# Kernel tuning notes

Hardware: AMD Instinct MI355X
Metric: run time of the kernel (lower is better)

Reference implementation:

```python
import jax, jax.numpy as jnp
import numpy as np
from math import gcd


def _get_start_index(length):
    if length <= 2:
        return 0
    return (length - 1) // 2


def setup_inputs() -> dict:
    key = jax.random.key(0)
    k1, k2 = jax.random.split(key)
    N = 8388608          # signal length (2^23 samples)
    F = 1023             # FIR taps
    x = jax.random.normal(k1, (N,), dtype=jnp.float32)
    filter_coeffs = jax.random.normal(k2, (F,), dtype=jnp.float32)
    return {"x": x, "up": 3, "down": 2, "filter_coeffs": filter_coeffs}


def reference(x, up, down, filter_coeffs):
    # Reduce the rational ratio (static Python ints)
    g = gcd(up, down)
    up = up // g
    down = down // g

    N = x.shape[0]
    F = filter_coeffs.shape[0]

    # Zero-stuff: x_up[::up] = up * x  -> length up*N
    x_up = jnp.zeros(up * N, dtype=x.dtype).at[::up].set(up * x)

    start = _get_start_index(F)
    out_len = (N * up) // down + bool((N * up) % down)

    if up == 1 and down == 1:
        return x_up[:out_len]

    # torch.conv1d(x_up, flip(h), padding=F-1) == full convolution np.convolve(x_up, h)
    full = jnp.convolve(x_up, filter_coeffs, mode="full")  # length up*N + F - 1
    x_out = full[start::down]
    return x_out[:out_len]
```

## Files before the change

### kernel.cpp

```cpp
#include <hip/hip_runtime.h>


typedef __attribute__((ext_vector_type(8))) short bf16x8;
typedef __attribute__((ext_vector_type(4))) float f32x4;

constexpr int SBLK = 4096;
constexpr int TPW  = 4;
constexpr int NQ   = 12;
constexpr int XSEG = 1072;
constexpr int AFN  = 3 * NQ * 64;

constexpr int SMEM_BYTES = 17152 + 36864;

__device__ __forceinline__ unsigned short f2bf(float f) {
    union { float f; unsigned int u; } c; c.f = f;
    unsigned int u = c.u;
    return (unsigned short)((u + 0x7FFFu + ((u >> 16) & 1u)) >> 16);
}
__device__ __forceinline__ int swz(int seg) { return seg ^ ((seg >> 3) & 7); }

__global__ __launch_bounds__(256)
void resample_mfma_kernel(const float* __restrict__ x,
                          const float* __restrict__ h,
                          float* __restrict__ out, int N)
{
    __shared__ __align__(16) char smem[SMEM_BYTES];
    unsigned short* xr = (unsigned short*)smem;
    uint4* afr  = (uint4*)(smem + 17152);
    float4* ob4 = (float4*)smem;

    const int tid = threadIdx.x;
    const int s0  = blockIdx.x * SBLK;
    const int GHI = 2 * s0 + 8363;

    for (int e = tid; e < AFN; e += 256) {
        const int r   = e / 768;
        const int rem = e - r * 768;
        const int q   = rem >> 6;
        const int le  = rem & 63;
        const int Tb  = 32 * q + 2 * (le & 15) + 8 * (le >> 4);
        unsigned int w[4];
        #pragma unroll
        for (int jp = 0; jp < 4; ++jp) {
            unsigned short half[2];
            #pragma unroll
            for (int u = 0; u < 2; ++u) {
                const int t   = Tb + 2 * jp + u - 32;
                const int hix = (r == 0) ? 3 * t - 2 : ((r == 1) ? 3 * t : 3 * t + 2);
                half[u] = (t >= 0 && hix >= 0 && hix < 1023) ? f2bf(3.0f * h[hix])
                                                             : (unsigned short)0;
            }
            w[jp] = (unsigned)half[0] | ((unsigned)half[1] << 16);
        }
        afr[e] = make_uint4(w[0], w[1], w[2], w[3]);
    }

    for (int st = tid; st < XSEG; st += 256) {
        const int g7 = GHI - 8 * st - 7;
        float f[8];
        if (g7 >= 0 && g7 + 7 < N) {
            const float4 lo = *reinterpret_cast<const float4*>(x + g7);
            const float4 hi = *reinterpret_cast<const float4*>(x + g7 + 4);
            f[0] = hi.w; f[1] = hi.z; f[2] = hi.y; f[3] = hi.x;
            f[4] = lo.w; f[5] = lo.z; f[6] = lo.y; f[7] = lo.x;
        } else {
            #pragma unroll
            for (int e = 0; e < 8; ++e) {
                const int idx = GHI - 8 * st - e;
                f[e] = (idx >= 0 && idx < N) ? x[idx] : 0.0f;
            }
        }
        uint4 w;
        w.x = (unsigned)f2bf(f[0]) | ((unsigned)f2bf(f[1]) << 16);
        w.y = (unsigned)f2bf(f[2]) | ((unsigned)f2bf(f[3]) << 16);
        w.z = (unsigned)f2bf(f[4]) | ((unsigned)f2bf(f[5]) << 16);
        w.w = (unsigned)f2bf(f[6]) | ((unsigned)f2bf(f[7]) << 16);
        *reinterpret_cast<uint4*>(xr + 8 * swz(st)) = w;
    }
    __syncthreads();

    const int wave = tid >> 6;
    const int lane = tid & 63;
    const int n    = lane & 15;
    const int quad = lane >> 4;

    f32x4 acc[TPW][3] = {};

    #pragma unroll
    for (int q = 0; q < NQ; ++q) {
        bf16x8 A[3];
        #pragma unroll
        for (int r = 0; r < 3; ++r)
            A[r] = __builtin_bit_cast(bf16x8, afr[(r * 12 + q) * 64 + lane]);
        #pragma unroll
        for (int jj = 0; jj < TPW; ++jj) {
            const int tile = wave * TPW + jj;
            const int seg  = 1020 - 64 * tile - 4 * n + 4 * q + quad;
            const bf16x8 B = __builtin_bit_cast(
                bf16x8, *reinterpret_cast<const uint4*>(xr + 8 * swz(seg)));
            #pragma unroll
            for (int r = 0; r < 3; ++r)
                acc[jj][r] = __builtin_amdgcn_mfma_f32_16x16x32_bf16(A[r], B, acc[jj][r], 0, 0, 0);
        }
    }

    __syncthreads();

    #pragma unroll
    for (int jj = 0; jj < TPW; ++jj) {
        const int T  = wave * TPW + jj;
        const int cb = (T * 64 + lane) * 3;
        float v[12];
        #pragma unroll
        for (int r = 0; r < 3; ++r)
            #pragma unroll
            for (int i = 0; i < 4; ++i)
                v[3 * i + r] = acc[jj][r][i];
        #pragma unroll
        for (int j = 0; j < 3; ++j)
            ob4[cb + j] = make_float4(v[4 * j], v[4 * j + 1], v[4 * j + 2], v[4 * j + 3]);
    }
    __syncthreads();

    const int obase = 3 * s0;
    #pragma unroll
    for (int it = 0; it < 12; ++it) {
        const int o   = it * 1024 + 4 * tid;
        const int T   = o / 768;
        const int w2  = o - 768 * T;
        const int nn  = w2 / 48;
        const int rm  = w2 - 48 * nn;
        const int qd  = rm / 12;
        const int dd  = rm - 12 * qd;
        const float4 val = ob4[(T * 64 + 16 * qd + nn) * 3 + (dd >> 2)];
        *reinterpret_cast<float4*>(out + obase + o) = val;
    }
}

extern "C" void kernel_launch(void* const* d_in, const int* in_sizes, int n_in,
                              void* d_out, int out_size, void* d_ws, size_t ws_size,
                              hipStream_t stream)
{
    const float* x = (const float*)d_in[0];
    const float* h = (const float*)d_in[3];
    float* out = (float*)d_out;

    const int N    = in_sizes[0];
    const int S    = out_size / 3;
    const int nblk = S / SBLK;

    resample_mfma_kernel<<<nblk, 256, 0, stream>>>(x, h, out, N);
}
```

Measured before the change: 118.5 us.

## Precompute filter fragments in a separate kernel and store outputs directly from registers

Moves the per-block construction of bf16 filter fragments into a small pre-kernel that writes them to the workspace, so the main kernel reads A fragments from global memory instead of rebuilding them in LDS every block. Shared memory drops to only the input tile, which allows more blocks per CU. The LDS-staged output transpose and its two barriers are replaced by direct float4 stores from accumulators, and the q loop is only partially unrolled. The trade-offs are an extra kernel launch, global/L2 reads of the fragments inside the MFMA loop, and less coalesced output stores.

```diff
diff --git a/kernel.cpp b/kernel.cpp
--- a/kernel.cpp
+++ b/kernel.cpp
@@ -10,8 +10,6 @@
 constexpr int XSEG = 1072;
 constexpr int AFN  = 3 * NQ * 64;
 
-constexpr int SMEM_BYTES = 17152 + 36864;
-
 __device__ __forceinline__ unsigned short f2bf(float f) {
     union { float f; unsigned int u; } c; c.f = f;
     unsigned int u = c.u;
@@ -20,40 +18,41 @@
 __device__ __forceinline__ int swz(int seg) { return seg ^ ((seg >> 3) & 7); }
 
 __global__ __launch_bounds__(256)
+void build_afr_kernel(const float* __restrict__ h, uint4* __restrict__ afr)
+{
+    const int e = blockIdx.x * 256 + threadIdx.x;
+    if (e >= AFN) return;
+    const int r   = e / 768;
+    const int rem = e - r * 768;
+    const int q   = rem >> 6;
+    const int le  = rem & 63;
+    const int Tb  = 32 * q + 2 * (le & 15) + 8 * (le >> 4);
+    unsigned int w[4];
+    #pragma unroll
+    for (int jp = 0; jp < 4; ++jp) {
+        unsigned short half[2];
+        #pragma unroll
+        for (int u = 0; u < 2; ++u) {
+            const int t   = Tb + 2 * jp + u - 32;
+            const int hix = (r == 0) ? 3 * t - 2 : ((r == 1) ? 3 * t : 3 * t + 2);
+            half[u] = (t >= 0 && hix >= 0 && hix < 1023) ? f2bf(3.0f * h[hix])
+                                                         : (unsigned short)0;
+        }
+        w[jp] = (unsigned)half[0] | ((unsigned)half[1] << 16);
+    }
+    afr[e] = make_uint4(w[0], w[1], w[2], w[3]);
+}
+
+__global__ __launch_bounds__(256)
 void resample_mfma_kernel(const float* __restrict__ x,
-                          const float* __restrict__ h,
+                          const uint4* __restrict__ afr,
                           float* __restrict__ out, int N)
 {
-    __shared__ __align__(16) char smem[SMEM_BYTES];
-    unsigned short* xr = (unsigned short*)smem;
-    uint4* afr  = (uint4*)(smem + 17152);
-    float4* ob4 = (float4*)smem;
+    __shared__ __align__(16) unsigned short xr[8576];
 
     const int tid = threadIdx.x;
     const int s0  = blockIdx.x * SBLK;
     const int GHI = 2 * s0 + 8363;
-
-    for (int e = tid; e < AFN; e += 256) {
-        const int r   = e / 768;
-        const int rem = e - r * 768;
-        const int q   = rem >> 6;
-        const int le  = rem & 63;
-        const int Tb  = 32 * q + 2 * (le & 15) + 8 * (le >> 4);
-        unsigned int w[4];
-        #pragma unroll
-        for (int jp = 0; jp < 4; ++jp) {
-            unsigned short half[2];
-            #pragma unroll
-            for (int u = 0; u < 2; ++u) {
-                const int t   = Tb + 2 * jp + u - 32;
-                const int hix = (r == 0) ? 3 * t - 2 : ((r == 1) ? 3 * t : 3 * t + 2);
-                half[u] = (t >= 0 && hix >= 0 && hix < 1023) ? f2bf(3.0f * h[hix])
-                                                             : (unsigned short)0;
-            }
-            w[jp] = (unsigned)half[0] | ((unsigned)half[1] << 16);
-        }
-        afr[e] = make_uint4(w[0], w[1], w[2], w[3]);
-    }
 
     for (int st = tid; st < XSEG; st += 256) {
         const int g7 = GHI - 8 * st - 7;
@@ -86,7 +85,7 @@
 
     f32x4 acc[TPW][3] = {};
 
-    #pragma unroll
+    #pragma unroll 2
     for (int q = 0; q < NQ; ++q) {
         bf16x8 A[3];
         #pragma unroll
@@ -104,36 +103,19 @@
         }
     }
 
-    __syncthreads();
-
     #pragma unroll
     for (int jj = 0; jj < TPW; ++jj) {
-        const int T  = wave * TPW + jj;
-        const int cb = (T * 64 + lane) * 3;
+        const int T = wave * TPW + jj;
         float v[12];
         #pragma unroll
         for (int r = 0; r < 3; ++r)
             #pragma unroll
             for (int i = 0; i < 4; ++i)
                 v[3 * i + r] = acc[jj][r][i];
-        #pragma unroll
-        for (int j = 0; j < 3; ++j)
-            ob4[cb + j] = make_float4(v[4 * j], v[4 * j + 1], v[4 * j + 2], v[4 * j + 3]);
-    }
-    __syncthreads();
-
-    const int obase = 3 * s0;
-    #pragma unroll
-    for (int it = 0; it < 12; ++it) {
-        const int o   = it * 1024 + 4 * tid;
-        const int T   = o / 768;
-        const int w2  = o - 768 * T;
-        const int nn  = w2 / 48;
-        const int rm  = w2 - 48 * nn;
-        const int qd  = rm / 12;
-        const int dd  = rm - 12 * qd;
-        const float4 val = ob4[(T * 64 + 16 * qd + nn) * 3 + (dd >> 2)];
-        *reinterpret_cast<float4*>(out + obase + o) = val;
+        float* po = out + 3 * s0 + 768 * T + 48 * n + 12 * quad;
+        *reinterpret_cast<float4*>(po)     = make_float4(v[0], v[1], v[2],  v[3]);
+        *reinterpret_cast<float4*>(po + 4) = make_float4(v[4], v[5], v[6],  v[7]);
+        *reinterpret_cast<float4*>(po + 8) = make_float4(v[8], v[9], v[10], v[11]);
     }
 }
 
@@ -144,10 +126,12 @@
     const float* x = (const float*)d_in[0];
     const float* h = (const float*)d_in[3];
     float* out = (float*)d_out;
+    uint4* afr = (uint4*)d_ws;
 
     const int N    = in_sizes[0];
     const int S    = out_size / 3;
     const int nblk = S / SBLK;
 
-    resample_mfma_kernel<<<nblk, 256, 0, stream>>>(x, h, out, N);
+    build_afr_kernel<<<(AFN + 255) / 256, 256, 0, stream>>>(h, afr);
+    resample_mfma_kernel<<<nblk, 256, 0, stream>>>(x, afr, out, N);
 }
```

After: 107.3 us. 1.1x faster.
